# Kernel optimization log

Measured on AMD Instinct MI355X. Metric: run time of the kernel, lower is better.

Reference implementation:

```python
import jax, jax.numpy as jnp
import numpy as np

B, S, D, H = 2, 2048, 1024, 16
DK = D // H  # 64
EPS = 1e-10
ROPE_BASE = 500000.0


def _rms_norm(x, w):
    # RMSNorm over last dim: w * x / sqrt(mean(x^2) + eps)
    return w * x * jax.lax.rsqrt(jnp.mean(x * x, axis=-1, keepdims=True) + EPS)


def _rope_tables(seq_len, dk):
    inv_freq = 1.0 / (ROPE_BASE ** (jnp.arange(0, dk, 2, dtype=jnp.float32) / dk))
    t = jnp.arange(seq_len, dtype=jnp.float32)
    freqs = jnp.outer(t, inv_freq)            # (S, dk/2)
    emb = jnp.concatenate([freqs, freqs], -1)  # (S, dk)
    return jnp.cos(emb), jnp.sin(emb)


def _rotate_half(x):
    x1, x2 = jnp.split(x, 2, axis=-1)
    return jnp.concatenate([-x2, x1], axis=-1)


def setup_inputs() -> dict:
    key = jax.random.key(0)
    ks = jax.random.split(key, 8)
    scale = 1.0 / np.sqrt(D)
    return {
        "q": jax.random.normal(ks[0], (B, S, D), jnp.float32),
        "k": jax.random.normal(ks[1], (B, S, D), jnp.float32),
        "v": jax.random.normal(ks[2], (B, S, D), jnp.float32),
        "Wq": jax.random.normal(ks[3], (D, D), jnp.float32) * scale,
        "Wk": jax.random.normal(ks[4], (D, D), jnp.float32) * scale,
        "Wv": jax.random.normal(ks[5], (D, D), jnp.float32) * scale,
        "Wo": jax.random.normal(ks[6], (D, D), jnp.float32) * scale,
        "q_norm_w": jnp.ones((DK,), jnp.float32) + 0.02 * jax.random.normal(ks[7], (DK,), jnp.float32),
        "k_norm_w": jnp.ones((DK,), jnp.float32),
    }


def reference(q, k, v, Wq, Wk, Wv, Wo, q_norm_w, k_norm_w):
    Bq, Sq, _ = q.shape
    # Projections (torch Linear: x @ W.T), split into heads -> (B, H, S, DK)
    def proj(x, W):
        return (x @ W.T).reshape(Bq, Sq, H, DK).transpose(0, 2, 1, 3)
    query, key_, value = proj(q, Wq), proj(k, Wk), proj(v, Wv)
    # Per-head QK RMSNorm
    query = _rms_norm(query, q_norm_w)
    key_ = _rms_norm(key_, k_norm_w)
    # RoPE
    cos, sin = _rope_tables(Sq, DK)  # (S, DK) each; broadcast over (B, H)
    query = query * cos + _rotate_half(query) * sin
    key_ = key_ * cos + _rotate_half(key_) * sin
    # Causal attention
    scale = 1.0 / np.sqrt(DK)
    scores = jnp.einsum("bhqd,bhkd->bhqk", query, key_) * scale
    causal = jnp.tril(jnp.ones((Sq, Sq), bool))
    scores = jnp.where(causal, scores, -jnp.inf)
    probs = jax.nn.softmax(scores, axis=-1)
    attn = jnp.einsum("bhqk,bhkd->bhqd", probs, value)
    # Merge heads and output projection
    attn = attn.transpose(0, 2, 1, 3).reshape(Bq, Sq, D)
    return attn @ Wo.T
```

## Files before the change

### kernel.cpp

```cpp
#include <hip/hip_runtime.h>
#include <hip/hip_bf16.h>
#include <math.h>

#define B_  2
#define S_  2048
#define D_  1024
#define H_  16
#define DK_ 64

typedef __attribute__((ext_vector_type(8))) short bf16x8;
typedef __attribute__((ext_vector_type(4))) float f32x4;
typedef __attribute__((ext_vector_type(4))) unsigned int u32x4;

#define MFMA_BF16(a, b, c) __builtin_amdgcn_mfma_f32_16x16x32_bf16((a), (b), (c), 0, 0, 0)

#define QSCALE 0.18033688011112042f
#define ROPE_L2 0.591611512f

__device__ __forceinline__ unsigned short f2bf(float f) {
  unsigned int u = __float_as_uint(f);
  u += 0x7FFFu + ((u >> 16) & 1u);
  return (unsigned short)(u >> 16);
}

__device__ __forceinline__ void gl_lds16(const void* g, void* l) {
  __builtin_amdgcn_global_load_lds(
      (const __attribute__((address_space(1))) void*)g,
      (__attribute__((address_space(3))) void*)l, 16, 0, 0);
}

__device__ __forceinline__ int lsw(int row, int col) {
  return row * 64 + ((((col) >> 3) ^ (row & 7)) << 3) + (col & 7);
}

__device__ __forceinline__ int vperm_inv(int c) {
  return (c & 32) | ((c & 8) << 1) | ((c & 4) << 1) | ((c & 16) >> 2);
}

__global__ __launch_bounds__(256)
void cvt_bf16(const float* __restrict__ q, const float* __restrict__ k,
              const float* __restrict__ v, const float* __restrict__ wq,
              const float* __restrict__ wk, const float* __restrict__ wv,
              const float* __restrict__ wo,
              unsigned short* __restrict__ qb, unsigned short* __restrict__ kb,
              unsigned short* __restrict__ vb, unsigned short* __restrict__ wqb,
              unsigned short* __restrict__ wkb, unsigned short* __restrict__ wvb,
              unsigned short* __restrict__ wob) {
  const float* src; unsigned short* dst; int n;
  switch (blockIdx.y) {
    case 0: src = q;  dst = qb;  n = B_ * S_ * D_; break;
    case 1: src = k;  dst = kb;  n = B_ * S_ * D_; break;
    case 2: src = v;  dst = vb;  n = B_ * S_ * D_; break;
    case 3: src = wq; dst = wqb; n = D_ * D_; break;
    case 4: src = wk; dst = wkb; n = D_ * D_; break;
    case 5: src = wv; dst = wvb; n = D_ * D_; break;
    default: src = wo; dst = wob; n = D_ * D_; break;
  }
  const int i = (blockIdx.x * 256 + threadIdx.x) * 4;
  if (i >= n) return;
  float4 val = *(const float4*)&src[i];
  ushort4 r4;
  r4.x = f2bf(val.x); r4.y = f2bf(val.y); r4.z = f2bf(val.z); r4.w = f2bf(val.w);
  *(ushort4*)&dst[i] = r4;
}

__global__ __launch_bounds__(256)
void gemm_qkv(const unsigned short* __restrict__ qa, const unsigned short* __restrict__ ka,
              const unsigned short* __restrict__ va,
              const unsigned short* __restrict__ wq, const unsigned short* __restrict__ wk,
              const unsigned short* __restrict__ wv,
              unsigned short* __restrict__ Qo, unsigned short* __restrict__ Ko,
              unsigned short* __restrict__ Vto,
              const float* __restrict__ qnw, const float* __restrict__ knw) {
  __shared__ unsigned short As[2][128 * 32];
  __shared__ unsigned short Bs[2][128 * 32];

  const int lin = blockIdx.x + (blockIdx.y << 3) + (blockIdx.z << 8);
  const int v_  = (lin & 7) * 96 + (lin >> 3);
  const int bx  = v_ & 7;
  const int panel = v_ >> 3;
  const int by  = panel & 31;
  const int z   = panel >> 5;

  const unsigned short* A = (z == 0) ? qa : (z == 1) ? ka : va;
  const unsigned short* W = (z == 0) ? wq : (z == 1) ? wk : wv;

  const int t = threadIdx.x, lane = t & 63, wave = t >> 6;
  const int l16 = lane & 15, quad = lane >> 4;
  const int wm = wave >> 1, wn = wave & 1;
  const int m0 = by * 128, j0 = bx * 128;

  f32x4 acc[4][4];
#pragma unroll
  for (int i = 0; i < 4; ++i)
#pragma unroll
    for (int j = 0; j < 4; ++j) acc[i][j] = (f32x4)(0.0f);

  auto stage = [&](int kb, int buf) {
#pragma unroll
    for (int i = 0; i < 2; ++i) {
      const int c  = (wave * 2 + i) * 64 + lane;
      const int r  = c >> 2;
      const int co = (c & 3) * 8;
      gl_lds16(&A[(size_t)(m0 + r) * D_ + kb + co], &As[buf][(wave * 2 + i) * 512]);
      gl_lds16(&W[(size_t)(j0 + r) * D_ + kb + co], &Bs[buf][(wave * 2 + i) * 512]);
    }
  };

  stage(0, 0);
  for (int kb = 0; kb < D_; kb += 32) {
    const int buf = (kb >> 5) & 1;
    __syncthreads();
    if (kb + 32 < D_) stage(kb + 32, buf ^ 1);

    bf16x8 af[4], bfr[4];
#pragma unroll
    for (int mi = 0; mi < 4; ++mi)
      af[mi] = *(const bf16x8*)&As[buf][(wm * 64 + mi * 16 + l16) * 32 + quad * 8];
#pragma unroll
    for (int ni = 0; ni < 4; ++ni)
      bfr[ni] = *(const bf16x8*)&Bs[buf][(wn * 64 + ni * 16 + l16) * 32 + quad * 8];
#pragma unroll
    for (int mi = 0; mi < 4; ++mi)
#pragma unroll
      for (int ni = 0; ni < 4; ++ni)
        acc[mi][ni] = MFMA_BF16(af[mi], bfr[ni], acc[mi][ni]);
  }

  const int h = bx * 2 + wn;
  if (z == 2) {
#pragma unroll
    for (int mi = 0; mi < 4; ++mi) {
      const int rowb = m0 + wm * 64 + mi * 16 + quad * 4;
      const int b = rowb >> 11, s0 = rowb & (S_ - 1);
      const int sp = (s0 & ~63) | vperm_inv(s0 & 63);
#pragma unroll
      for (int ni = 0; ni < 4; ++ni) {
        const int dk = ni * 16 + l16;
        const unsigned int u0 =
            (unsigned int)f2bf(acc[mi][ni][0]) | ((unsigned int)f2bf(acc[mi][ni][1]) << 16);
        const unsigned int u1 =
            (unsigned int)f2bf(acc[mi][ni][2]) | ((unsigned int)f2bf(acc[mi][ni][3]) << 16);
        *(uint2*)&Vto[((size_t)((b * H_ + h) * DK_ + dk)) * S_ + sp] = make_uint2(u0, u1);
      }
    }
  } else {
    unsigned short* out = (z == 0) ? Qo : Ko;
    const float* nw = (z == 0) ? qnw : knw;
    const float sc  = (z == 0) ? QSCALE : 1.0f;
    float wv_[4];
#pragma unroll
    for (int ni = 0; ni < 4; ++ni) wv_[ni] = nw[ni * 16 + l16];
    const float invA = exp2f(-(float)l16 * ROPE_L2);
    const float invB = exp2f(-(float)(16 + l16) * ROPE_L2);
#pragma unroll
    for (int mi = 0; mi < 4; ++mi) {
#pragma unroll
      for (int r = 0; r < 4; ++r) {
        const int rowg = m0 + wm * 64 + mi * 16 + quad * 4 + r;
        const int b = rowg >> 11, s = rowg & (S_ - 1);
        float ss = 0.f;
#pragma unroll
        for (int ni = 0; ni < 4; ++ni) ss += acc[mi][ni][r] * acc[mi][ni][r];
#pragma unroll
        for (int m = 1; m < 16; m <<= 1) ss += __shfl_xor(ss, m);
        const float rms = rsqrtf(ss * (1.0f / DK_) + 1e-10f);
        float xn[4];
#pragma unroll
        for (int ni = 0; ni < 4; ++ni) xn[ni] = wv_[ni] * acc[mi][ni][r] * rms;
        const float fA = (float)s * invA, fB = (float)s * invB;
        const float cA = __cosf(fA) * sc, sA = __sinf(fA) * sc;
        const float cB = __cosf(fB) * sc, sB = __sinf(fB) * sc;
        float o0 = xn[0] * cA - xn[2] * sA;
        float o1 = xn[1] * cB - xn[3] * sB;
        float o2 = xn[2] * cA + xn[0] * sA;
        float o3 = xn[3] * cB + xn[1] * sB;
        const size_t base = ((size_t)(b * H_ + h) * S_ + s) * DK_;
        out[base +  0 + l16] = f2bf(o0);
        out[base + 16 + l16] = f2bf(o1);
        out[base + 32 + l16] = f2bf(o2);
        out[base + 48 + l16] = f2bf(o3);
      }
    }
  }
}

__global__ __launch_bounds__(256)
void flash3(const unsigned short* __restrict__ Q, const unsigned short* __restrict__ K,
            const unsigned short* __restrict__ Vt, unsigned short* __restrict__ Oa) {
  __shared__ unsigned short Ks[2][64 * 64];
  __shared__ unsigned short Vs[2][64 * 64];
  const int bx = blockIdx.x;
  const int idx = bx >> 5;
  const int qt = (idx < 16) ? idx : (47 - idx);
  const int bh = bx & 31;
  const int t = threadIdx.x, lane = t & 63, wave = t >> 6;
  const int l16 = lane & 15, quad = lane >> 4;
  const size_t hb = (size_t)bh * S_ * DK_;
  const unsigned short* Qh  = Q + hb;
  const unsigned short* Kh  = K + hb;
  const unsigned short* Vth = Vt + hb;

  bf16x8 qf[2];
#pragma unroll
  for (int ks = 0; ks < 2; ++ks)
    qf[ks] = *(const bf16x8*)
      &Qh[(size_t)(qt * 64 + wave * 16 + l16) * DK_ + ks * 32 + quad * 8];

  bf16x8 ones;
#pragma unroll
  for (int j = 0; j < 8; ++j) ones[j] = (short)0x3F80;

  f32x4 o[4], lacc;
  lacc = (f32x4)(0.0f);
#pragma unroll
  for (int ni = 0; ni < 4; ++ni) o[ni] = (f32x4)(0.0f);

  auto stage = [&](int kt, int bufi) {
#pragma unroll
    for (int i = 0; i < 2; ++i) {
      const int rbase = wave * 16 + i * 8;
      const int r = rbase + (lane >> 3);
      const int c = ((lane & 7) ^ (r & 7)) * 8;
      gl_lds16(&Kh[(size_t)(kt * 64 + r) * DK_ + c], &Ks[bufi][rbase * 64]);
      gl_lds16(&Vth[(size_t)r * S_ + kt * 64 + c], &Vs[bufi][rbase * 64]);
    }
  };

  const int nkt = qt + 1;
  stage(0, 0);
  for (int kt = 0; kt < nkt; ++kt) {
    const int buf = kt & 1;
    __syncthreads();
    if (kt + 1 < nkt) stage(kt + 1, buf ^ 1);

    f32x4 sv[4];
#pragma unroll
    for (int kvi = 0; kvi < 4; ++kvi) sv[kvi] = (f32x4)(0.0f);
#pragma unroll
    for (int ks = 0; ks < 2; ++ks) {
      bf16x8 ak[4];
#pragma unroll
      for (int kvi = 0; kvi < 4; ++kvi)
        ak[kvi] = *(const bf16x8*)&Ks[buf][lsw(kvi * 16 + l16, ks * 32 + quad * 8)];
      __builtin_amdgcn_s_setprio(1);
#pragma unroll
      for (int kvi = 0; kvi < 4; ++kvi)
        sv[kvi] = MFMA_BF16(ak[kvi], qf[ks], sv[kvi]);
      __builtin_amdgcn_s_setprio(0);
    }

    unsigned int pw[4][2];
    if (kt == qt) {
      const int qg = qt * 64 + wave * 16 + l16;
#pragma unroll
      for (int kvi = 0; kvi < 4; ++kvi) {
        float e[4];
#pragma unroll
        for (int r = 0; r < 4; ++r) {
          float x = sv[kvi][r];
          if ((kt * 64 + kvi * 16 + quad * 4 + r) > qg) x = -INFINITY;
          e[r] = exp2f(x);
        }
        pw[kvi][0] = (__float_as_uint(e[1]) & 0xFFFF0000u) | (__float_as_uint(e[0]) >> 16);
        pw[kvi][1] = (__float_as_uint(e[3]) & 0xFFFF0000u) | (__float_as_uint(e[2]) >> 16);
      }
    } else {
#pragma unroll
      for (int kvi = 0; kvi < 4; ++kvi) {
        float e[4];
#pragma unroll
        for (int r = 0; r < 4; ++r) e[r] = exp2f(sv[kvi][r]);
        pw[kvi][0] = (__float_as_uint(e[1]) & 0xFFFF0000u) | (__float_as_uint(e[0]) >> 16);
        pw[kvi][1] = (__float_as_uint(e[3]) & 0xFFFF0000u) | (__float_as_uint(e[2]) >> 16);
      }
    }

    bf16x8 ap[2];
#pragma unroll
    for (int ks = 0; ks < 2; ++ks) {
      u32x4 aw;
      aw.x = pw[2 * ks][0];
      aw.y = pw[2 * ks][1];
      aw.z = pw[2 * ks + 1][0];
      aw.w = pw[2 * ks + 1][1];
      ap[ks] = __builtin_bit_cast(bf16x8, aw);
    }

#pragma unroll
    for (int ks = 0; ks < 2; ++ks) {
      bf16x8 bv[4];
#pragma unroll
      for (int ni = 0; ni < 4; ++ni)
        bv[ni] = *(const bf16x8*)&Vs[buf][lsw(ni * 16 + l16, ks * 32 + quad * 8)];
      __builtin_amdgcn_s_setprio(1);
#pragma unroll
      for (int ni = 0; ni < 4; ++ni)
        o[ni] = MFMA_BF16(ap[ks], bv[ni], o[ni]);
      lacc = MFMA_BF16(ap[ks], ones, lacc);
      __builtin_amdgcn_s_setprio(0);
    }
  }

  const int b = bh >> 4, h = bh & 15;
#pragma unroll
  for (int r = 0; r < 4; ++r) {
    const int srow = qt * 64 + wave * 16 + quad * 4 + r;
    const float linv = 1.0f / lacc[r];
#pragma unroll
    for (int ni = 0; ni < 4; ++ni)
      Oa[((size_t)(b * S_ + srow) * H_ + h) * DK_ + ni * 16 + l16] =
          f2bf(o[ni][r] * linv);
  }
}

__global__ __launch_bounds__(256)
void gemm_out(const unsigned short* __restrict__ A, const unsigned short* __restrict__ W,
              float* __restrict__ out) {
  __shared__ unsigned short As[2][128 * 32];
  __shared__ unsigned short Bs[2][128 * 32];
  const int lin = blockIdx.x + (blockIdx.y << 3);
  const int v_  = (lin & 7) * 32 + (lin >> 3);
  const int bx  = v_ & 7;
  const int by  = v_ >> 3;

  const int t = threadIdx.x, lane = t & 63, wave = t >> 6;
  const int l16 = lane & 15, quad = lane >> 4;
  const int wm = wave >> 1, wn = wave & 1;
  const int m0 = by * 128, j0 = bx * 128;

  f32x4 acc[4][4];
#pragma unroll
  for (int i = 0; i < 4; ++i)
#pragma unroll
    for (int j = 0; j < 4; ++j) acc[i][j] = (f32x4)(0.0f);

  auto stage = [&](int kb, int buf) {
#pragma unroll
    for (int i = 0; i < 2; ++i) {
      const int c  = (wave * 2 + i) * 64 + lane;
      const int r  = c >> 2;
      const int co = (c & 3) * 8;
      gl_lds16(&A[(size_t)(m0 + r) * D_ + kb + co], &As[buf][(wave * 2 + i) * 512]);
      gl_lds16(&W[(size_t)(j0 + r) * D_ + kb + co], &Bs[buf][(wave * 2 + i) * 512]);
    }
  };

  stage(0, 0);
  for (int kb = 0; kb < D_; kb += 32) {
    const int buf = (kb >> 5) & 1;
    __syncthreads();
    if (kb + 32 < D_) stage(kb + 32, buf ^ 1);

    bf16x8 af[4], bfr[4];
#pragma unroll
    for (int mi = 0; mi < 4; ++mi)
      af[mi] = *(const bf16x8*)&As[buf][(wm * 64 + mi * 16 + l16) * 32 + quad * 8];
#pragma unroll
    for (int ni = 0; ni < 4; ++ni)
      bfr[ni] = *(const bf16x8*)&Bs[buf][(wn * 64 + ni * 16 + l16) * 32 + quad * 8];
#pragma unroll
    for (int mi = 0; mi < 4; ++mi)
#pragma unroll
      for (int ni = 0; ni < 4; ++ni)
        acc[mi][ni] = MFMA_BF16(af[mi], bfr[ni], acc[mi][ni]);
  }

#pragma unroll
  for (int mi = 0; mi < 4; ++mi) {
    const int rowb = m0 + wm * 64 + mi * 16 + quad * 4;
#pragma unroll
    for (int ni = 0; ni < 4; ++ni) {
      const int col = j0 + wn * 64 + ni * 16 + l16;
#pragma unroll
      for (int r = 0; r < 4; ++r)
        out[(size_t)(rowb + r) * D_ + col] = acc[mi][ni][r];
    }
  }
}

extern "C" void kernel_launch(void* const* d_in, const int* in_sizes, int n_in,
                              void* d_out, int out_size, void* d_ws, size_t ws_size,
                              hipStream_t stream) {
  (void)in_sizes; (void)n_in; (void)out_size; (void)ws_size;
  const float* q  = (const float*)d_in[0];
  const float* k  = (const float*)d_in[1];
  const float* v  = (const float*)d_in[2];
  const float* Wq = (const float*)d_in[3];
  const float* Wk = (const float*)d_in[4];
  const float* Wv = (const float*)d_in[5];
  const float* Wo = (const float*)d_in[6];
  const float* qw = (const float*)d_in[7];
  const float* kw = (const float*)d_in[8];

  char* ws = (char*)d_ws;
  const size_t MB = 1u << 20;
  unsigned short* qb  = (unsigned short*)(ws + 0 * MB);
  unsigned short* kb  = (unsigned short*)(ws + 8 * MB);
  unsigned short* vb  = (unsigned short*)(ws + 16 * MB);
  unsigned short* wqb = (unsigned short*)(ws + 24 * MB);
  unsigned short* wkb = (unsigned short*)(ws + 26 * MB);
  unsigned short* wvb = (unsigned short*)(ws + 28 * MB);
  unsigned short* wob = (unsigned short*)(ws + 30 * MB);
  unsigned short* Qb  = (unsigned short*)(ws + 32 * MB);
  unsigned short* Kb  = (unsigned short*)(ws + 40 * MB);
  unsigned short* Vtb = (unsigned short*)(ws + 48 * MB);
  unsigned short* Ab  = (unsigned short*)(ws + 56 * MB);

  cvt_bf16<<<dim3(4096, 7), 256, 0, stream>>>(q, k, v, Wq, Wk, Wv, Wo,
                                              qb, kb, vb, wqb, wkb, wvb, wob);

  gemm_qkv<<<dim3(D_ / 128, (B_ * S_) / 128, 3), 256, 0, stream>>>(
      qb, kb, vb, wqb, wkb, wvb, Qb, Kb, Vtb, qw, kw);

  flash3<<<1024, 256, 0, stream>>>(Qb, Kb, Vtb, Ab);

  gemm_out<<<dim3(D_ / 128, (B_ * S_) / 128), 256, 0, stream>>>(Ab, wob, (float*)d_out);
}
```

Baseline: 206.5 us.

## Rewrite QKV projection GEMM with 256x256 tiles, swizzled LDS and phased pipeline

The QKV GEMM moves from 128x128 tiles with 4 waves and K-step 32 to 256x256 tiles with 8 waves and K-step 64. It adds an XOR-swizzled LDS layout (via lsw) and a four-phase schedule that interleaves global-to-LDS staging with MFMA bursts under explicit barriers, waitcnts and setprio. The aim is more operand reuse per LDS load, fewer bank conflicts and better overlap of loads with compute. The grid shrinks to 192 blocks, which may underfill the 256 CUs of the MI355X. The larger tile also raises register and LDS pressure.

Result: no change. 210.4 us (+1.9%).

```diff
diff --git a/kernel.cpp b/kernel.cpp
--- a/kernel.cpp
+++ b/kernel.cpp
@@ -64,7 +64,7 @@
   *(ushort4*)&dst[i] = r4;
 }
 
-__global__ __launch_bounds__(256)
+__global__ __launch_bounds__(512, 2)
 void gemm_qkv(const unsigned short* __restrict__ qa, const unsigned short* __restrict__ ka,
               const unsigned short* __restrict__ va,
               const unsigned short* __restrict__ wq, const unsigned short* __restrict__ wk,
@@ -72,75 +72,127 @@
               unsigned short* __restrict__ Qo, unsigned short* __restrict__ Ko,
               unsigned short* __restrict__ Vto,
               const float* __restrict__ qnw, const float* __restrict__ knw) {
-  __shared__ unsigned short As[2][128 * 32];
-  __shared__ unsigned short Bs[2][128 * 32];
-
-  const int lin = blockIdx.x + (blockIdx.y << 3) + (blockIdx.z << 8);
-  const int v_  = (lin & 7) * 96 + (lin >> 3);
-  const int bx  = v_ & 7;
-  const int panel = v_ >> 3;
-  const int by  = panel & 31;
-  const int z   = panel >> 5;
+  __shared__ unsigned short As[2][16384];
+  __shared__ unsigned short Bs[2][16384];
+
+  const int lin = blockIdx.x + (blockIdx.y << 2) + (blockIdx.z << 6);
+  const int v_  = (lin & 7) * 24 + (lin >> 3);
+  const int bxn = v_ & 3;
+  const int r2  = v_ >> 2;
+  const int by  = r2 & 15;
+  const int z   = r2 >> 4;
 
   const unsigned short* A = (z == 0) ? qa : (z == 1) ? ka : va;
   const unsigned short* W = (z == 0) ? wq : (z == 1) ? wk : wv;
 
-  const int t = threadIdx.x, lane = t & 63, wave = t >> 6;
+  const int tid = threadIdx.x, lane = tid & 63, wave = tid >> 6;
   const int l16 = lane & 15, quad = lane >> 4;
-  const int wm = wave >> 1, wn = wave & 1;
-  const int m0 = by * 128, j0 = bx * 128;
-
-  f32x4 acc[4][4];
-#pragma unroll
-  for (int i = 0; i < 4; ++i)
+  const int wm = wave >> 2, wn2 = wave & 3;
+  const int m0 = by * 256, j0 = bxn * 256;
+
+  f32x4 acc[8][4];
+#pragma unroll
+  for (int i = 0; i < 8; ++i)
 #pragma unroll
     for (int j = 0; j < 4; ++j) acc[i][j] = (f32x4)(0.0f);
 
-  auto stage = [&](int kb, int buf) {
-#pragma unroll
-    for (int i = 0; i < 2; ++i) {
-      const int c  = (wave * 2 + i) * 64 + lane;
-      const int r  = c >> 2;
-      const int co = (c & 3) * 8;
-      gl_lds16(&A[(size_t)(m0 + r) * D_ + kb + co], &As[buf][(wave * 2 + i) * 512]);
-      gl_lds16(&W[(size_t)(j0 + r) * D_ + kb + co], &Bs[buf][(wave * 2 + i) * 512]);
+  auto stageA = [&](int tile, int h) {
+    const int kb = tile * 64, R0 = m0 + h * 128;
+#pragma unroll
+    for (int j = 0; j < 2; ++j) {
+      const int c = j * 512 + tid;
+      const int r = c >> 3;
+      const int co = (((c & 7) ^ (r & 7)) << 3);
+      gl_lds16(&A[(size_t)(R0 + r) * D_ + kb + co],
+               &As[tile & 1][h * 8192 + ((c & ~63) << 3)]);
     }
   };
-
-  stage(0, 0);
-  for (int kb = 0; kb < D_; kb += 32) {
-    const int buf = (kb >> 5) & 1;
-    __syncthreads();
-    if (kb + 32 < D_) stage(kb + 32, buf ^ 1);
-
-    bf16x8 af[4], bfr[4];
-#pragma unroll
-    for (int mi = 0; mi < 4; ++mi)
-      af[mi] = *(const bf16x8*)&As[buf][(wm * 64 + mi * 16 + l16) * 32 + quad * 8];
-#pragma unroll
-    for (int ni = 0; ni < 4; ++ni)
-      bfr[ni] = *(const bf16x8*)&Bs[buf][(wn * 64 + ni * 16 + l16) * 32 + quad * 8];
-#pragma unroll
-    for (int mi = 0; mi < 4; ++mi)
-#pragma unroll
-      for (int ni = 0; ni < 4; ++ni)
-        acc[mi][ni] = MFMA_BF16(af[mi], bfr[ni], acc[mi][ni]);
-  }
-
-  const int h = bx * 2 + wn;
+  auto stageB = [&](int tile, int h) {
+    const int kb = tile * 64, R0 = j0 + h * 128;
+#pragma unroll
+    for (int j = 0; j < 2; ++j) {
+      const int c = j * 512 + tid;
+      const int r = c >> 3;
+      const int co = (((c & 7) ^ (r & 7)) << 3);
+      gl_lds16(&W[(size_t)(R0 + r) * D_ + kb + co],
+               &Bs[tile & 1][h * 8192 + ((c & ~63) << 3)]);
+    }
+  };
+
+#define PHASE(BUF, QH, MFA, MFB, STAGES)                                        \
+  do {                                                                          \
+    bf16x8 af0[2], af1[2];                                                      \
+    _Pragma("unroll")                                                           \
+    for (int ks = 0; ks < 2; ++ks) {                                            \
+      af0[ks] = *(const bf16x8*)&As[BUF][(QH) * 8192 +                          \
+                    lsw(((MFA) & 3) * 32 + wm * 16 + l16, ks * 32 + quad * 8)]; \
+      af1[ks] = *(const bf16x8*)&As[BUF][(QH) * 8192 +                          \
+                    lsw(((MFB) & 3) * 32 + wm * 16 + l16, ks * 32 + quad * 8)]; \
+    }                                                                           \
+    STAGES;                                                                     \
+    __builtin_amdgcn_s_barrier();                                               \
+    asm volatile("s_waitcnt lgkmcnt(0)" ::: "memory");                          \
+    __builtin_amdgcn_sched_barrier(0);                                          \
+    __builtin_amdgcn_s_setprio(1);                                              \
+    _Pragma("unroll")                                                           \
+    for (int ks = 0; ks < 2; ++ks) {                                            \
+      _Pragma("unroll")                                                         \
+      for (int nf = 0; nf < 4; ++nf) {                                          \
+        acc[MFA][nf] = MFMA_BF16(af0[ks], bfr[nf][ks], acc[MFA][nf]);           \
+        acc[MFB][nf] = MFMA_BF16(af1[ks], bfr[nf][ks], acc[MFB][nf]);           \
+      }                                                                         \
+    }                                                                           \
+    __builtin_amdgcn_s_setprio(0);                                              \
+  } while (0)
+
+  const int NT = D_ / 64;
+  stageA(0, 0); stageA(0, 1); stageB(0, 0); stageB(0, 1); stageA(1, 0);
+  asm volatile("s_waitcnt vmcnt(2)" ::: "memory");
+  __builtin_amdgcn_s_barrier();
+
+  for (int tt = 0; tt < NT; ++tt) {
+    const int buf = tt & 1;
+    bf16x8 bfr[4][2];
+#pragma unroll
+    for (int nf = 0; nf < 4; ++nf)
+#pragma unroll
+      for (int ks = 0; ks < 2; ++ks)
+        bfr[nf][ks] = *(const bf16x8*)&Bs[buf][(wn2 >> 1) * 8192 +
+            lsw((wn2 & 1) * 64 + nf * 16 + l16, ks * 32 + quad * 8)];
+
+    PHASE(buf, 0, 0, 1,
+          if (tt + 1 < NT) { stageB(tt + 1, 0); stageA(tt + 1, 1); });
+    __builtin_amdgcn_s_barrier();
+    PHASE(buf, 0, 2, 3,
+          if (tt + 1 < NT) { stageB(tt + 1, 1); });
+    __builtin_amdgcn_s_barrier();
+    PHASE(buf, 1, 4, 5,
+          if (tt + 2 < NT) { stageA(tt + 2, 0); });
+    __builtin_amdgcn_s_barrier();
+    PHASE(buf, 1, 6, 7, );
+    if (tt <= NT - 3) {
+      asm volatile("s_waitcnt vmcnt(2)" ::: "memory");
+    } else {
+      asm volatile("s_waitcnt vmcnt(0)" ::: "memory");
+    }
+    __builtin_amdgcn_s_barrier();
+  }
+#undef PHASE
+
+  const int h = bxn * 4 + wn2;
   if (z == 2) {
 #pragma unroll
-    for (int mi = 0; mi < 4; ++mi) {
-      const int rowb = m0 + wm * 64 + mi * 16 + quad * 4;
+    for (int mf = 0; mf < 8; ++mf) {
+      const int rowb = m0 + mf * 32 + wm * 16 + quad * 4;
       const int b = rowb >> 11, s0 = rowb & (S_ - 1);
       const int sp = (s0 & ~63) | vperm_inv(s0 & 63);
 #pragma unroll
-      for (int ni = 0; ni < 4; ++ni) {
-        const int dk = ni * 16 + l16;
+      for (int nf = 0; nf < 4; ++nf) {
+        const int dk = nf * 16 + l16;
         const unsigned int u0 =
-            (unsigned int)f2bf(acc[mi][ni][0]) | ((unsigned int)f2bf(acc[mi][ni][1]) << 16);
+            (unsigned int)f2bf(acc[mf][nf][0]) | ((unsigned int)f2bf(acc[mf][nf][1]) << 16);
         const unsigned int u1 =
-            (unsigned int)f2bf(acc[mi][ni][2]) | ((unsigned int)f2bf(acc[mi][ni][3]) << 16);
+            (unsigned int)f2bf(acc[mf][nf][2]) | ((unsigned int)f2bf(acc[mf][nf][3]) << 16);
         *(uint2*)&Vto[((size_t)((b * H_ + h) * DK_ + dk)) * S_ + sp] = make_uint2(u0, u1);
       }
     }
@@ -150,24 +202,24 @@
     const float sc  = (z == 0) ? QSCALE : 1.0f;
     float wv_[4];
 #pragma unroll
-    for (int ni = 0; ni < 4; ++ni) wv_[ni] = nw[ni * 16 + l16];
+    for (int nf = 0; nf < 4; ++nf) wv_[nf] = nw[nf * 16 + l16];
     const float invA = exp2f(-(float)l16 * ROPE_L2);
     const float invB = exp2f(-(float)(16 + l16) * ROPE_L2);
 #pragma unroll
-    for (int mi = 0; mi < 4; ++mi) {
+    for (int mf = 0; mf < 8; ++mf) {
 #pragma unroll
       for (int r = 0; r < 4; ++r) {
-        const int rowg = m0 + wm * 64 + mi * 16 + quad * 4 + r;
+        const int rowg = m0 + mf * 32 + wm * 16 + quad * 4 + r;
         const int b = rowg >> 11, s = rowg & (S_ - 1);
         float ss = 0.f;
 #pragma unroll
-        for (int ni = 0; ni < 4; ++ni) ss += acc[mi][ni][r] * acc[mi][ni][r];
+        for (int nf = 0; nf < 4; ++nf) ss += acc[mf][nf][r] * acc[mf][nf][r];
 #pragma unroll
         for (int m = 1; m < 16; m <<= 1) ss += __shfl_xor(ss, m);
         const float rms = rsqrtf(ss * (1.0f / DK_) + 1e-10f);
         float xn[4];
 #pragma unroll
-        for (int ni = 0; ni < 4; ++ni) xn[ni] = wv_[ni] * acc[mi][ni][r] * rms;
+        for (int nf = 0; nf < 4; ++nf) xn[nf] = wv_[nf] * acc[mf][nf][r] * rms;
         const float fA = (float)s * invA, fB = (float)s * invB;
         const float cA = __cosf(fA) * sc, sA = __sinf(fA) * sc;
         const float cB = __cosf(fB) * sc, sB = __sinf(fB) * sc;
@@ -410,7 +462,7 @@
   cvt_bf16<<<dim3(4096, 7), 256, 0, stream>>>(q, k, v, Wq, Wk, Wv, Wo,
                                               qb, kb, vb, wqb, wkb, wvb, wob);
 
-  gemm_qkv<<<dim3(D_ / 128, (B_ * S_) / 128, 3), 256, 0, stream>>>(
+  gemm_qkv<<<dim3(4, 16, 3), 512, 0, stream>>>(
       qb, kb, vb, wqb, wkb, wvb, Qb, Kb, Vtb, qw, kw);
 
   flash3<<<1024, 256, 0, stream>>>(Qb, Kb, Vtb, Ab);
```

## Software-pipeline flash attention so QK^T of next tile overlaps PV of previous

Applied to the files above, without the earlier changes.

Restructures the attention inner loop so that the QK^T product and softmax for tile kt are issued alongside the PV product for tile kt-1, using two ping-pong probability register sets. V gets a third LDS buffer because V tiles must stay live one iteration longer than K tiles. The aim is to hide exp/pack latency behind MFMA work. It raises register pressure and LDS use, which may reduce occupancy.

Measured after the change: 203.4 us. No clear change (-1.5%).

```diff
diff --git a/kernel.cpp b/kernel.cpp
--- a/kernel.cpp
+++ b/kernel.cpp
@@ -189,7 +189,7 @@
 void flash3(const unsigned short* __restrict__ Q, const unsigned short* __restrict__ K,
             const unsigned short* __restrict__ Vt, unsigned short* __restrict__ Oa) {
   __shared__ unsigned short Ks[2][64 * 64];
-  __shared__ unsigned short Vs[2][64 * 64];
+  __shared__ unsigned short Vs[3][64 * 64];
   const int bx = blockIdx.x;
   const int idx = bx >> 5;
   const int qt = (idx < 16) ? idx : (47 - idx);
@@ -216,25 +216,21 @@
 #pragma unroll
   for (int ni = 0; ni < 4; ++ni) o[ni] = (f32x4)(0.0f);
 
-  auto stage = [&](int kt, int bufi) {
+  auto stage = [&](int kt, int kb_, int vb_) {
 #pragma unroll
     for (int i = 0; i < 2; ++i) {
       const int rbase = wave * 16 + i * 8;
       const int r = rbase + (lane >> 3);
       const int c = ((lane & 7) ^ (r & 7)) * 8;
-      gl_lds16(&Kh[(size_t)(kt * 64 + r) * DK_ + c], &Ks[bufi][rbase * 64]);
-      gl_lds16(&Vth[(size_t)r * S_ + kt * 64 + c], &Vs[bufi][rbase * 64]);
-    }
-  };
-
-  const int nkt = qt + 1;
-  stage(0, 0);
-  for (int kt = 0; kt < nkt; ++kt) {
+      gl_lds16(&Kh[(size_t)(kt * 64 + r) * DK_ + c], &Ks[kb_][rbase * 64]);
+      gl_lds16(&Vth[(size_t)r * S_ + kt * 64 + c], &Vs[vb_][rbase * 64]);
+    }
+  };
+
+  f32x4 sv[4];
+
+  auto qkt = [&](int kt) {
     const int buf = kt & 1;
-    __syncthreads();
-    if (kt + 1 < nkt) stage(kt + 1, buf ^ 1);
-
-    f32x4 sv[4];
 #pragma unroll
     for (int kvi = 0; kvi < 4; ++kvi) sv[kvi] = (f32x4)(0.0f);
 #pragma unroll
@@ -249,8 +245,9 @@
         sv[kvi] = MFMA_BF16(ak[kvi], qf[ks], sv[kvi]);
       __builtin_amdgcn_s_setprio(0);
     }
-
-    unsigned int pw[4][2];
+  };
+
+  auto smx = [&](int kt, unsigned int (&pw)[4][2]) {
     if (kt == qt) {
       const int qg = qt * 64 + wave * 16 + l16;
 #pragma unroll
@@ -275,7 +272,9 @@
         pw[kvi][1] = (__float_as_uint(e[3]) & 0xFFFF0000u) | (__float_as_uint(e[2]) >> 16);
       }
     }
-
+  };
+
+  auto pv = [&](const unsigned int (&pw)[4][2], int vb_) {
     bf16x8 ap[2];
 #pragma unroll
     for (int ks = 0; ks < 2; ++ks) {
@@ -286,13 +285,12 @@
       aw.w = pw[2 * ks + 1][1];
       ap[ks] = __builtin_bit_cast(bf16x8, aw);
     }
-
 #pragma unroll
     for (int ks = 0; ks < 2; ++ks) {
       bf16x8 bv[4];
 #pragma unroll
       for (int ni = 0; ni < 4; ++ni)
-        bv[ni] = *(const bf16x8*)&Vs[buf][lsw(ni * 16 + l16, ks * 32 + quad * 8)];
+        bv[ni] = *(const bf16x8*)&Vs[vb_][lsw(ni * 16 + l16, ks * 32 + quad * 8)];
       __builtin_amdgcn_s_setprio(1);
 #pragma unroll
       for (int ni = 0; ni < 4; ++ni)
@@ -300,6 +298,38 @@
       lacc = MFMA_BF16(ap[ks], ones, lacc);
       __builtin_amdgcn_s_setprio(0);
     }
+  };
+
+  const int nkt = qt + 1;
+  unsigned int pwA[4][2], pwB[4][2];
+
+  stage(0, 0, 0);
+  __syncthreads();
+  if (nkt > 1) stage(1, 1, 1);
+  qkt(0);
+  smx(0, pwA);
+
+  int kt = 1;
+  for (; kt + 1 < nkt; kt += 2) {
+    __syncthreads();
+    stage(kt + 1, (kt + 1) & 1, (kt + 1) % 3);
+    qkt(kt);
+    pv(pwA, (kt - 1) % 3);
+    smx(kt, pwB);
+    __syncthreads();
+    if (kt + 2 < nkt) stage(kt + 2, (kt + 2) & 1, (kt + 2) % 3);
+    qkt(kt + 1);
+    pv(pwB, kt % 3);
+    smx(kt + 1, pwA);
+  }
+  if (kt < nkt) {
+    __syncthreads();
+    qkt(kt);
+    pv(pwA, (kt - 1) % 3);
+    smx(kt, pwB);
+    pv(pwB, kt % 3);
+  } else {
+    pv(pwA, (nkt - 1) % 3);
   }
 
   const int b = bh >> 4, h = bh & 15;
```
